# Kernel optimization log

Measured on AMD Instinct MI355X. Metric: run time of the kernel, lower is better.

Reference implementation:

```python
import jax, jax.numpy as jnp
import numpy as np

B, D, L, T, K = 16, 256, 256, 1000, 3
DW, DC = 4, 2  # dim_w, dim_c
CH = 8         # ConvSwishBlock out channels (10 = 1 start + 1 end + 8)


def swish(x):
    return x * jax.nn.sigmoid(x)


def setup_inputs() -> dict:
    key = jax.random.key(0)
    ks = jax.random.split(key, 12)
    # durations ~ U[1,6] per phone -> sum ~ 3.5*L ~ 896 <= T
    durations = 1.0 + 5.0 * jax.random.uniform(ks[0], (B, L), dtype=jnp.float32)
    phoneme = jax.random.normal(ks[1], (B, D, L), dtype=jnp.float32)
    # True = padded phone position
    phone_len = L - (jnp.arange(B) % 4) * 16
    phoneme_mask = (jnp.arange(L)[None, :] >= phone_len[:, None])[:, None, :]
    durations = jnp.where(phoneme_mask[:, 0, :], 0.0, durations)
    s = 0.02
    p = {
        'proj_w_W': s * jax.random.normal(ks[2], (D, D)), 'proj_w_b': jnp.zeros((D,)),
        'conv_w_W': s * jax.random.normal(ks[3], (CH, D, K)), 'conv_w_b': jnp.zeros((CH,)),
        'mlp_w_W': s * jax.random.normal(ks[4], (2 + CH, DW)), 'mlp_w_b': jnp.zeros((DW,)),
        'lin_w_W': s * jax.random.normal(ks[5], (D * DW, D)), 'lin_w_b': jnp.zeros((D,)),
        'proj_c_W': s * jax.random.normal(ks[6], (D, D)), 'proj_c_b': jnp.zeros((D,)),
        'conv_c_W': s * jax.random.normal(ks[7], (CH, D, K)), 'conv_c_b': jnp.zeros((CH,)),
        'mlp_c_W': s * jax.random.normal(ks[8], (2 + CH, DC)), 'mlp_c_b': jnp.zeros((DC,)),
        'lin_c_W': s * jax.random.normal(ks[9], (DW * DC, D)), 'lin_c_b': jnp.zeros((D,)),
    }
    return {'durations': durations, 'phoneme': phoneme, 'phoneme_mask': phoneme_mask, **p}


def _conv_branch(x, phone_pad, projW, projb, convW, convb):
    # x: (B, D, L). 1x1 conv projection, then K-wide 'same' conv to CH channels, swish, mask.
    x = jnp.einsum('od,bdl->bol', projW, x) + projb[None, :, None]
    h = jax.lax.conv_general_dilated(x, convW, (1,), 'SAME',
                                     dimension_numbers=('NCH', 'OIH', 'NCH'))
    h = swish(h + convb[None, :, None])
    h = jnp.where(phone_pad[:, None, :], 0.0, h)
    return h.transpose(0, 2, 1)  # (B, L, CH)


def _forward(durations, phoneme, phoneme_mask,
             proj_w_W, proj_w_b, conv_w_W, conv_w_b, mlp_w_W, mlp_w_b, lin_w_W, lin_w_b,
             proj_c_W, proj_c_b, conv_c_W, conv_c_b, mlp_c_W, mlp_c_b, lin_c_W, lin_c_b):
    phone_pad = phoneme_mask[:, 0, :]                       # (B, L) True = pad
    frame_len = jnp.clip(jnp.round(jnp.sum(durations, -1)), 0, T).astype(jnp.int32)
    frame_pad = jnp.arange(T)[None, :] >= frame_len[:, None]  # (B, T) True = pad
    attn_pad = frame_pad[:, :, None] | phone_pad[:, None, :]  # (B, T, L)

    sd = jnp.cumsum(durations, -1)                          # (B, L) cumulative end times
    sk = sd - durations                                     # (B, L) start times
    t = jnp.arange(1, T + 1, dtype=durations.dtype)
    S = jnp.where(attn_pad, 0.0, t[None, :, None] - sk[:, None, :])                    # (B,T,L)
    E = jnp.where(attn_pad, 0.0, jnp.broadcast_to(sd[:, None, :], attn_pad.shape)
                  - sk[:, None, :])                                                    # (B,T,L)

    # W branch: per-(frame, phone) attention weights over phones
    h_w = _conv_branch(phoneme, phone_pad, proj_w_W, proj_w_b, conv_w_W, conv_w_b)     # (B,L,CH)
    feat_w = jnp.concatenate(
        [S[..., None], E[..., None], jnp.broadcast_to(h_w[:, None], (B, T, L, CH))], -1)
    w = swish(feat_w @ mlp_w_W + mlp_w_b)                   # (B, T, L, DW)
    w = jnp.where(phone_pad[:, None, :, None], -jnp.inf, w)
    w = jax.nn.softmax(w, axis=2)                           # softmax over phones
    w = jnp.where(frame_pad[:, :, None, None], 0.0, w)

    # C branch: auxiliary per-(frame, phone) context
    h_c = _conv_branch(phoneme, phone_pad, proj_c_W, proj_c_b, conv_c_W, conv_c_b)
    feat_c = jnp.concatenate(
        [S[..., None], E[..., None], jnp.broadcast_to(h_c[:, None], (B, T, L, CH))], -1)
    c = swish(feat_c @ mlp_c_W + mlp_c_b)                   # (B, T, L, DC)

    # combine: wh = einsum over phones with phoneme features, wc with c matrix
    wh = jnp.einsum('btnq,bnh->btqh', w, phoneme.transpose(0, 2, 1))  # (B,T,DW,D)
    wh = wh.reshape(B, T, DW * D) @ lin_w_W + lin_w_b                 # (B,T,D)
    wc = jnp.einsum('btnq,btnp->btqp', w, c)                          # (B,T,DW,DC)
    wc = wc.reshape(B, T, DW * DC) @ lin_c_W + lin_c_b                # (B,T,D)
    return wh + wc


def reference(durations, phoneme, phoneme_mask,
              proj_w_W, proj_w_b, conv_w_W, conv_w_b, mlp_w_W, mlp_w_b, lin_w_W, lin_w_b,
              proj_c_W, proj_c_b, conv_c_W, conv_c_b, mlp_c_W, mlp_c_b, lin_c_W, lin_c_b):
    return _forward(durations, phoneme, phoneme_mask,
                    proj_w_W, proj_w_b, conv_w_W, conv_w_b, mlp_w_W, mlp_w_b, lin_w_W, lin_w_b,
                    proj_c_W, proj_c_b, conv_c_W, conv_c_b, mlp_c_W, mlp_c_b, lin_c_W, lin_c_b)
```

## Files before the change

kernel.cpp:

```cpp
#include <hip/hip_runtime.h>


typedef short v8s __attribute__((ext_vector_type(8)));
typedef float f4 __attribute__((ext_vector_type(4)));

__device__ __forceinline__ float bf2f(unsigned short h) {
  return __uint_as_float(((unsigned int)h) << 16);
}
__device__ __forceinline__ unsigned short f2bf(float f) {
  unsigned int u = __float_as_uint(f);
  u = (u + 0x7FFFu + ((u >> 16) & 1u)) >> 16;
  return (unsigned short)u;
}
__device__ __forceinline__ float swishf(float x) {
  return x * __builtin_amdgcn_rcpf(1.f + __expf(-x));
}

__global__ __launch_bounds__(256) void k_prep(
    const float* __restrict__ dur, const float* __restrict__ ph,
    const float* __restrict__ liWw,
    const float* __restrict__ cvWw, const float* __restrict__ pjWw,
    const float* __restrict__ pjbw,
    const float* __restrict__ cvWc, const float* __restrict__ pjWc,
    const float* __restrict__ pjbc,
    float* __restrict__ sk, int* __restrict__ frame_len,
    unsigned short* __restrict__ Mb, float* __restrict__ bK,
    unsigned short* __restrict__ LWT, unsigned short* __restrict__ phT) {
  __shared__ float sm[32 * 33];
  int blk = blockIdx.x, tid = threadIdx.x;
  if (blk < 16) {
    int b = blk, l = tid;
    float d = dur[b * 256 + l];
    sm[l] = d;
    __syncthreads();
    for (int off = 1; off < 256; off <<= 1) {
      float v = (l >= off) ? sm[l - off] : 0.f;
      __syncthreads();
      sm[l] += v;
      __syncthreads();
    }
    sk[b * 256 + l] = sm[l] - d;
    if (l == 255) {
      int fl = (int)rintf(sm[255]);
      frame_len[b] = min(max(fl, 0), 1000);
    }
  } else if (blk < 64) {
    int x = blk - 16;
    int br = x / 24, ck = x % 24;
    int ch = ck / 3, k = ck % 3;
    const float* convW = br ? cvWc : cvWw;
    const float* projW = br ? pjWc : pjWw;
    const float* projb = br ? pjbc : pjbw;
    int d = tid;
    float acc = 0.f;
    for (int o = 0; o < 256; o++)
      acc += convW[ch * 768 + o * 3 + k] * projW[o * 256 + d];
    Mb[(br * 24 + ck) * 256 + d] = f2bf(acc);
    if (d == 0) {
      float bb = 0.f;
      for (int o = 0; o < 256; o++)
        bb += convW[ch * 768 + o * 3 + k] * projb[o];
      bK[br * 24 + ck] = bb;
    }
  } else if (blk < 320) {
    int idx = blk - 64;
    int kt = idx & 31, ot = idx >> 5;
    int tx = tid & 31, ty = tid >> 5;
#pragma unroll
    for (int r = 0; r < 4; r++) {
      int row = ty + r * 8;
      sm[row * 33 + tx] = liWw[(size_t)(kt * 32 + row) * 256 + ot * 32 + tx];
    }
    __syncthreads();
#pragma unroll
    for (int r = 0; r < 4; r++) {
      int row = ty + r * 8;
      LWT[(size_t)(ot * 32 + row) * 1024 + kt * 32 + tx] =
          f2bf(sm[tx * 33 + row]);
    }
  } else {
    int idx = blk - 320;
    int ht = idx & 7, lt = (idx >> 3) & 7, b = idx >> 6;
    int tx = tid & 31, ty = tid >> 5;
#pragma unroll
    for (int r = 0; r < 4; r++) {
      int row = ty + r * 8;
      sm[row * 33 + tx] =
          ph[(size_t)b * 65536 + (size_t)(ht * 32 + row) * 256 + lt * 32 + tx];
    }
    __syncthreads();
#pragma unroll
    for (int r = 0; r < 4; r++) {
      int row = ty + r * 8;
      phT[(size_t)b * 65536 + (size_t)(lt * 32 + row) * 256 + ht * 32 + tx] =
          f2bf(sm[tx * 33 + row]);
    }
  }
}

__global__ __launch_bounds__(256) void k_conv(
    const unsigned short* __restrict__ phT, const unsigned short* __restrict__ Mb,
    const float* __restrict__ bK, const float* __restrict__ cvbw,
    const float* __restrict__ cvbc, const float* __restrict__ dur,
    float* __restrict__ hw, float* __restrict__ hc) {
  __shared__ float C[256 * 49];
  int b = blockIdx.x;
  int tid = threadIdx.x, wave = tid >> 6, lane = tid & 63;
  int quad = lane >> 4, col = lane & 15;
  int l0 = wave * 64;
  const unsigned short* Ab = phT + (size_t)b * 65536;
  f4 acc[4][3] = {};
#pragma unroll
  for (int k0 = 0; k0 < 256; k0 += 32) {
    v8s af[4], bf[3];
#pragma unroll
    for (int lt = 0; lt < 4; lt++)
      af[lt] = *(const v8s*)(Ab + (size_t)(l0 + lt * 16 + col) * 256 + k0 + quad * 8);
#pragma unroll
    for (int ct = 0; ct < 3; ct++)
      bf[ct] = *(const v8s*)(Mb + (size_t)(ct * 16 + col) * 256 + k0 + quad * 8);
#pragma unroll
    for (int lt = 0; lt < 4; lt++)
#pragma unroll
      for (int ct = 0; ct < 3; ct++)
        acc[lt][ct] = __builtin_amdgcn_mfma_f32_16x16x32_bf16(af[lt], bf[ct],
                                                              acc[lt][ct], 0, 0, 0);
  }
#pragma unroll
  for (int lt = 0; lt < 4; lt++)
#pragma unroll
    for (int ct = 0; ct < 3; ct++)
#pragma unroll
      for (int r = 0; r < 4; r++)
        C[(l0 + lt * 16 + quad * 4 + r) * 49 + ct * 16 + col] = acc[lt][ct][r];
  __syncthreads();
  int l = tid;
  float dv = dur[b * 256 + l];
  bool vld = (dv != 0.f);
#pragma unroll
  for (int br = 0; br < 2; br++) {
    const float* convb = br ? cvbc : cvbw;
    float* dst = br ? hc : hw;
#pragma unroll
    for (int ch = 0; ch < 8; ch++) {
      int ck = br * 24 + ch * 3;
      float v = convb[ch] + bK[ck + 1] + C[l * 49 + ck + 1];
      if (l > 0) v += bK[ck + 0] + C[(l - 1) * 49 + ck + 0];
      if (l < 255) v += bK[ck + 2] + C[(l + 1) * 49 + ck + 2];
      v = swishf(v);
      dst[((size_t)(b * 256 + l)) * 8 + ch] = vld ? v : 0.f;
    }
  }
}

__global__ __launch_bounds__(256) void k_wG(
    const unsigned short* __restrict__ LWT, const unsigned short* __restrict__ phT,
    const float* __restrict__ dur, const float* __restrict__ sk,
    const int* __restrict__ frame_len, const float* __restrict__ hw,
    const float* __restrict__ hc, const float* __restrict__ mlpWw,
    const float* __restrict__ mlpbw, const float* __restrict__ mlpWc,
    const float* __restrict__ mlpbc, unsigned short* __restrict__ G,
    unsigned short* __restrict__ wout, float* __restrict__ wcout) {
  __shared__ __align__(16) char smem[15360];
  int blk = blockIdx.x;
  int tid = threadIdx.x, wave = tid >> 6, lane = tid & 63;
  if (blk < 512) {
    int x = blk & 7, q = (blk >> 3) & 3, b = blk >> 5;
    int o0 = (x >> 1) * 64, l0 = (x & 1) * 128;
    int quad = lane >> 4, col = lane & 15;
    unsigned short* Asm = (unsigned short*)smem;
    unsigned short* Bsm = Asm + 64 * 40;
    int arow = wave * 16 + (lane >> 2);
    int aseg = lane & 3;
    const unsigned short* Ag = LWT + (size_t)(o0 + arow) * 1024 + q * 256 + aseg * 8;
    unsigned short* Al = Asm + arow * 40 + aseg * 8;
    int brow = wave * 32 + (lane >> 2);
    const unsigned short* Bg0 =
        phT + (size_t)b * 65536 + (size_t)(l0 + brow) * 256 + aseg * 8;
    const unsigned short* Bg1 = Bg0 + 16 * 256;
    unsigned short* Bl0 = Bsm + brow * 40 + aseg * 8;
    unsigned short* Bl1 = Bl0 + 16 * 40;
    int wm = (wave & 1) * 32, wn = (wave >> 1) * 64;
    f4 acc[2][4] = {};
    uint4 ra = *(const uint4*)Ag;
    uint4 rb0 = *(const uint4*)Bg0;
    uint4 rb1 = *(const uint4*)Bg1;
    for (int k0 = 0; k0 < 256; k0 += 32) {
      __syncthreads();
      *(uint4*)Al = ra;
      *(uint4*)Bl0 = rb0;
      *(uint4*)Bl1 = rb1;
      __syncthreads();
      if (k0 + 32 < 256) {
        ra = *(const uint4*)(Ag + k0 + 32);
        rb0 = *(const uint4*)(Bg0 + k0 + 32);
        rb1 = *(const uint4*)(Bg1 + k0 + 32);
      }
      v8s af[2], bf[4];
#pragma unroll
      for (int mt = 0; mt < 2; mt++)
        af[mt] = *(const v8s*)(Asm + (wm + mt * 16 + col) * 40 + quad * 8);
#pragma unroll
      for (int nt = 0; nt < 4; nt++)
        bf[nt] = *(const v8s*)(Bsm + (wn + nt * 16 + col) * 40 + quad * 8);
#pragma unroll
      for (int mt = 0; mt < 2; mt++)
#pragma unroll
        for (int nt = 0; nt < 4; nt++)
          acc[mt][nt] = __builtin_amdgcn_mfma_f32_16x16x32_bf16(af[mt], bf[nt],
                                                                acc[mt][nt], 0, 0, 0);
    }
    int quad2 = lane >> 4, col2 = lane & 15;
#pragma unroll
    for (int mt = 0; mt < 2; mt++)
#pragma unroll
      for (int nt = 0; nt < 4; nt++)
#pragma unroll
        for (int r = 0; r < 4; r++) {
          int orow = o0 + wm + mt * 16 + quad2 * 4 + r;
          int lcol = l0 + wn + nt * 16 + col2;
          G[(size_t)b * 262144 + (size_t)orow * 1024 + q * 256 + lcol] =
              f2bf(acc[mt][nt][r]);
        }
  } else {
    int idx = blk - 512;
    int b = idx >> 5;
    int tbase = (idx & 31) * 32 + wave * 8;
    int l0 = lane * 4;
    float mw[40], mbw[4], mc[20], mbc[2];
#pragma unroll
    for (int i = 0; i < 40; i++) mw[i] = mlpWw[i];
#pragma unroll
    for (int i = 0; i < 4; i++) mbw[i] = mlpbw[i];
#pragma unroll
    for (int i = 0; i < 20; i++) mc[i] = mlpWc[i];
#pragma unroll
    for (int i = 0; i < 2; i++) mbc[i] = mlpbc[i];
    float4 dv4 = *(const float4*)&dur[b * 256 + l0];
    float4 sk4 = *(const float4*)&sk[b * 256 + l0];
    float dv[4] = {dv4.x, dv4.y, dv4.z, dv4.w};
    float skv[4] = {sk4.x, sk4.y, sk4.z, sk4.w};
    bool val[4];
#pragma unroll
    for (int j = 0; j < 4; j++) val[j] = (dv[j] != 0.f);
    float hwv[4][8], hcv[4][8];
#pragma unroll
    for (int j = 0; j < 4; j++) {
      float4 a0 = *(const float4*)&hw[((size_t)(b * 256 + l0 + j)) * 8];
      float4 a1 = *(const float4*)&hw[((size_t)(b * 256 + l0 + j)) * 8 + 4];
      float4 c0 = *(const float4*)&hc[((size_t)(b * 256 + l0 + j)) * 8];
      float4 c1 = *(const float4*)&hc[((size_t)(b * 256 + l0 + j)) * 8 + 4];
      hwv[j][0] = a0.x; hwv[j][1] = a0.y; hwv[j][2] = a0.z; hwv[j][3] = a0.w;
      hwv[j][4] = a1.x; hwv[j][5] = a1.y; hwv[j][6] = a1.z; hwv[j][7] = a1.w;
      hcv[j][0] = c0.x; hcv[j][1] = c0.y; hcv[j][2] = c0.z; hcv[j][3] = c0.w;
      hcv[j][4] = c1.x; hcv[j][5] = c1.y; hcv[j][6] = c1.z; hcv[j][7] = c1.w;
    }
    float basew[4][4], basec[4][2];
#pragma unroll
    for (int j = 0; j < 4; j++) {
#pragma unroll
      for (int q = 0; q < 4; q++) {
        float a = mbw[q] + dv[j] * mw[4 + q];
#pragma unroll
        for (int ch = 0; ch < 8; ch++) a += hwv[j][ch] * mw[(2 + ch) * 4 + q];
        basew[j][q] = a;
      }
#pragma unroll
      for (int p = 0; p < 2; p++) {
        float a = mbc[p] + dv[j] * mc[2 + p];
#pragma unroll
        for (int ch = 0; ch < 8; ch++) a += hcv[j][ch] * mc[(2 + ch) * 2 + p];
        basec[j][p] = a;
      }
    }
    int fl = frame_len[b];
    for (int i = 0; i < 8; i++) {
      int t = tbase + i;
      if (t >= 1000) break;
      size_t wbase = ((size_t)(b * 1000 + t)) * 1024;
      if (t >= fl) {
        ushort4 z = {0, 0, 0, 0};
#pragma unroll
        for (int q = 0; q < 4; q++) *(ushort4*)(wout + wbase + q * 256 + l0) = z;
        if (lane == 0) {
          float4 fz = {0.f, 0.f, 0.f, 0.f};
          *(float4*)(wcout + ((size_t)(b * 1000 + t)) * 8) = fz;
          *(float4*)(wcout + ((size_t)(b * 1000 + t)) * 8 + 4) = fz;
        }
        continue;
      }
      float S[4];
#pragma unroll
      for (int j = 0; j < 4; j++) S[j] = (float)(t + 1) - skv[j];
      float lg[4][4];
#pragma unroll
      for (int j = 0; j < 4; j++)
#pragma unroll
        for (int q = 0; q < 4; q++)
          lg[j][q] = val[j] ? swishf(basew[j][q] + S[j] * mw[q]) : -INFINITY;
      float mx[4];
#pragma unroll
      for (int q = 0; q < 4; q++) {
        float v = fmaxf(fmaxf(lg[0][q], lg[1][q]), fmaxf(lg[2][q], lg[3][q]));
#pragma unroll
        for (int m = 1; m < 64; m <<= 1) v = fmaxf(v, __shfl_xor(v, m));
        mx[q] = v;
      }
      float e[4][4];
#pragma unroll
      for (int j = 0; j < 4; j++)
#pragma unroll
        for (int q = 0; q < 4; q++)
          e[j][q] = val[j] ? __expf(lg[j][q] - mx[q]) : 0.f;
      float inv[4];
#pragma unroll
      for (int q = 0; q < 4; q++) {
        float v = (e[0][q] + e[1][q]) + (e[2][q] + e[3][q]);
#pragma unroll
        for (int m = 1; m < 64; m <<= 1) v += __shfl_xor(v, m);
        inv[q] = __builtin_amdgcn_rcpf(v);
      }
      float w[4][4];
#pragma unroll
      for (int q = 0; q < 4; q++) {
        ushort4 o4;
        w[0][q] = e[0][q] * inv[q]; w[1][q] = e[1][q] * inv[q];
        w[2][q] = e[2][q] * inv[q]; w[3][q] = e[3][q] * inv[q];
        o4.x = f2bf(w[0][q]); o4.y = f2bf(w[1][q]);
        o4.z = f2bf(w[2][q]); o4.w = f2bf(w[3][q]);
        *(ushort4*)(wout + wbase + q * 256 + l0) = o4;
      }
      float cp[4][2];
#pragma unroll
      for (int j = 0; j < 4; j++)
#pragma unroll
        for (int p = 0; p < 2; p++)
          cp[j][p] = swishf(basec[j][p] + S[j] * mc[p]);
      float pr[8];
#pragma unroll
      for (int q = 0; q < 4; q++)
#pragma unroll
        for (int p = 0; p < 2; p++) {
          float v = w[0][q] * cp[0][p] + w[1][q] * cp[1][p] +
                    w[2][q] * cp[2][p] + w[3][q] * cp[3][p];
#pragma unroll
          for (int m = 1; m < 64; m <<= 1) v += __shfl_xor(v, m);
          pr[q * 2 + p] = v;
        }
      if (lane == 0) {
        float4 lo = {pr[0], pr[1], pr[2], pr[3]};
        float4 hi = {pr[4], pr[5], pr[6], pr[7]};
        *(float4*)(wcout + ((size_t)(b * 1000 + t)) * 8) = lo;
        *(float4*)(wcout + ((size_t)(b * 1000 + t)) * 8 + 4) = hi;
      }
    }
  }
}

__global__ __launch_bounds__(256) void k_gemmF(const unsigned short* __restrict__ wbuf,
                                               const unsigned short* __restrict__ G,
                                               const float* __restrict__ lwb,
                                               const float* __restrict__ lcb,
                                               const float* __restrict__ LC,
                                               const float* __restrict__ wc,
                                               float* __restrict__ out) {
  int b = blockIdx.y;
  int t0 = (blockIdx.x >> 1) * 64;
  int o0 = (blockIdx.x & 1) * 128;
  int tid = threadIdx.x, wave = tid >> 6, lane = tid & 63;
  int quad = lane >> 4, col = lane & 15;
  __shared__ __align__(16) unsigned short Asm[64 * 40];
  __shared__ __align__(16) unsigned short Bsm[128 * 40];
  __shared__ float bias_s[128];
  __shared__ float lcs[8][128];
  __shared__ float wcs[64][8];

  for (int i = tid; i < 128; i += 256) bias_s[i] = lwb[o0 + i] + lcb[o0 + i];
  for (int i = tid; i < 1024; i += 256)
    lcs[i >> 7][i & 127] = LC[(i >> 7) * 256 + o0 + (i & 127)];
  for (int i = tid; i < 512; i += 256) {
    int r = i >> 3, j = i & 7;
    int t = t0 + r;
    wcs[r][j] = (t < 1000) ? wc[((size_t)(b * 1000 + t)) * 8 + j] : 0.f;
  }

  int arow = wave * 16 + (lane >> 2);
  int aseg = lane & 3;
  const unsigned short* Ag =
      wbuf + (size_t)b * 1024000 + (size_t)(t0 + arow) * 1024 + aseg * 8;
  unsigned short* Al = Asm + arow * 40 + aseg * 8;
  int brow = wave * 32 + (lane >> 2);
  const unsigned short* Bg0 =
      G + (size_t)b * 262144 + (size_t)(o0 + brow) * 1024 + aseg * 8;
  const unsigned short* Bg1 = Bg0 + 16 * 1024;
  unsigned short* Bl0 = Bsm + brow * 40 + aseg * 8;
  unsigned short* Bl1 = Bl0 + 16 * 40;

  int wm = (wave & 1) * 32, wn = (wave >> 1) * 64;
  f4 acc[2][4] = {};
  uint4 ra = *(const uint4*)Ag;
  uint4 rb0 = *(const uint4*)Bg0;
  uint4 rb1 = *(const uint4*)Bg1;
  for (int k0 = 0; k0 < 1024; k0 += 32) {
    __syncthreads();
    *(uint4*)Al = ra;
    *(uint4*)Bl0 = rb0;
    *(uint4*)Bl1 = rb1;
    __syncthreads();
    if (k0 + 32 < 1024) {
      ra = *(const uint4*)(Ag + k0 + 32);
      rb0 = *(const uint4*)(Bg0 + k0 + 32);
      rb1 = *(const uint4*)(Bg1 + k0 + 32);
    }
    v8s af[2], bf[4];
#pragma unroll
    for (int mt = 0; mt < 2; mt++)
      af[mt] = *(const v8s*)(Asm + (wm + mt * 16 + col) * 40 + quad * 8);
#pragma unroll
    for (int nt = 0; nt < 4; nt++)
      bf[nt] = *(const v8s*)(Bsm + (wn + nt * 16 + col) * 40 + quad * 8);
#pragma unroll
    for (int mt = 0; mt < 2; mt++)
#pragma unroll
      for (int nt = 0; nt < 4; nt++)
        acc[mt][nt] = __builtin_amdgcn_mfma_f32_16x16x32_bf16(af[mt], bf[nt],
                                                              acc[mt][nt], 0, 0, 0);
  }
#pragma unroll
  for (int mt = 0; mt < 2; mt++)
#pragma unroll
    for (int r = 0; r < 4; r++) {
      int lrow = wm + mt * 16 + quad * 4 + r;
      int trow = t0 + lrow;
      if (trow < 1000) {
        float wcl[8];
        float4 wa = *(const float4*)&wcs[lrow][0];
        float4 wb = *(const float4*)&wcs[lrow][4];
        wcl[0] = wa.x; wcl[1] = wa.y; wcl[2] = wa.z; wcl[3] = wa.w;
        wcl[4] = wb.x; wcl[5] = wb.y; wcl[6] = wb.z; wcl[7] = wb.w;
#pragma unroll
        for (int nt = 0; nt < 4; nt++) {
          int oc = wn + nt * 16 + col;
          float v = acc[mt][nt][r] + bias_s[oc];
#pragma unroll
          for (int jj = 0; jj < 8; jj++) v = fmaf(wcl[jj], lcs[jj][oc], v);
          out[((size_t)(b * 1000 + trow)) * 256 + o0 + oc] = v;
        }
      }
    }
}

extern "C" void kernel_launch(void* const* d_in, const int* in_sizes, int n_in,
                              void* d_out, int out_size, void* d_ws, size_t ws_size,
                              hipStream_t stream) {
  const float* dur  = (const float*)d_in[0];
  const float* ph   = (const float*)d_in[1];
  const float* pjWw = (const float*)d_in[3];
  const float* pjbw = (const float*)d_in[4];
  const float* cvWw = (const float*)d_in[5];
  const float* cvbw = (const float*)d_in[6];
  const float* mlWw = (const float*)d_in[7];
  const float* mlbw = (const float*)d_in[8];
  const float* liWw = (const float*)d_in[9];
  const float* libw = (const float*)d_in[10];
  const float* pjWc = (const float*)d_in[11];
  const float* pjbc = (const float*)d_in[12];
  const float* cvWc = (const float*)d_in[13];
  const float* cvbc = (const float*)d_in[14];
  const float* mlWc = (const float*)d_in[15];
  const float* mlbc = (const float*)d_in[16];
  const float* liWc = (const float*)d_in[17];
  const float* libc = (const float*)d_in[18];
  float* out = (float*)d_out;

  float* f = (float*)d_ws;
  size_t o = 0;
  float* sk = f + o;            o += 4096;
  int* fl = (int*)(f + o);      o += 16;
  float* bK = f + o;            o += 64;
  unsigned short* Mb = (unsigned short*)(f + o); o += 6144;
  float* hw = f + o;            o += 16 * 256 * 8;
  float* hc = f + o;            o += 16 * 256 * 8;
  float* wc = f + o;            o += 16 * 1000 * 8;
  unsigned short* wbuf = (unsigned short*)(f + o); o += 8224768;
  unsigned short* G    = (unsigned short*)(f + o); o += 2097152;
  unsigned short* phT  = (unsigned short*)(f + o); o += 524288;
  unsigned short* LWT  = (unsigned short*)(f + o); o += 131072;

  k_prep<<<1344, 256, 0, stream>>>(dur, ph, liWw, cvWw, pjWw, pjbw, cvWc, pjWc,
                                   pjbc, sk, fl, Mb, bK, LWT, phT);
  k_conv<<<16, 256, 0, stream>>>(phT, Mb, bK, cvbw, cvbc, dur, hw, hc);
  k_wG<<<1024, 256, 0, stream>>>(LWT, phT, dur, sk, fl, hw, hc, mlWw, mlbw,
                                 mlWc, mlbc, G, wbuf, wc);
  k_gemmF<<<dim3(32, 16), 256, 0, stream>>>(wbuf, G, libw, libc, liWc, wc, out);
}
```

Baseline: 187.9 us.

## Fuse softmax weight generation into final GEMM, merge conv with G GEMM

The softmax attention weights are now computed per t-tile inside the final GEMM kernel and staged as unnormalized bf16 exponentials in shared memory. Per-row normalization is applied after each q-slice GEMM, so the large bf16 weight buffer is no longer written to and read back from global memory. The conv kernel and the G GEMM are merged into one launch, which cuts the launch count and lets the two run concurrently. In exchange, each of the two o-tiles for a given t-range recomputes the softmax, and the kernel uses more shared memory and issues more syncs per block.

```diff
diff --git a/kernel.cpp b/kernel.cpp
--- a/kernel.cpp
+++ b/kernel.cpp
@@ -98,76 +98,68 @@
   }
 }
 
-__global__ __launch_bounds__(256) void k_conv(
+__global__ __launch_bounds__(256) void k_convG(
     const unsigned short* __restrict__ phT, const unsigned short* __restrict__ Mb,
     const float* __restrict__ bK, const float* __restrict__ cvbw,
     const float* __restrict__ cvbc, const float* __restrict__ dur,
-    float* __restrict__ hw, float* __restrict__ hc) {
-  __shared__ float C[256 * 49];
-  int b = blockIdx.x;
+    const unsigned short* __restrict__ LWT,
+    float* __restrict__ hw, float* __restrict__ hc,
+    unsigned short* __restrict__ G) {
+  __shared__ __align__(16) char smem[50176];
+  int blk = blockIdx.x;
   int tid = threadIdx.x, wave = tid >> 6, lane = tid & 63;
   int quad = lane >> 4, col = lane & 15;
-  int l0 = wave * 64;
-  const unsigned short* Ab = phT + (size_t)b * 65536;
-  f4 acc[4][3] = {};
-#pragma unroll
-  for (int k0 = 0; k0 < 256; k0 += 32) {
-    v8s af[4], bf[3];
+  if (blk < 16) {
+    float* C = (float*)smem;
+    int b = blk;
+    int l0 = wave * 64;
+    const unsigned short* Ab = phT + (size_t)b * 65536;
+    f4 acc[4][3] = {};
+#pragma unroll
+    for (int k0 = 0; k0 < 256; k0 += 32) {
+      v8s af[4], bf[3];
+#pragma unroll
+      for (int lt = 0; lt < 4; lt++)
+        af[lt] = *(const v8s*)(Ab + (size_t)(l0 + lt * 16 + col) * 256 + k0 + quad * 8);
+#pragma unroll
+      for (int ct = 0; ct < 3; ct++)
+        bf[ct] = *(const v8s*)(Mb + (size_t)(ct * 16 + col) * 256 + k0 + quad * 8);
+#pragma unroll
+      for (int lt = 0; lt < 4; lt++)
+#pragma unroll
+        for (int ct = 0; ct < 3; ct++)
+          acc[lt][ct] = __builtin_amdgcn_mfma_f32_16x16x32_bf16(af[lt], bf[ct],
+                                                                acc[lt][ct], 0, 0, 0);
+    }
 #pragma unroll
     for (int lt = 0; lt < 4; lt++)
-      af[lt] = *(const v8s*)(Ab + (size_t)(l0 + lt * 16 + col) * 256 + k0 + quad * 8);
-#pragma unroll
-    for (int ct = 0; ct < 3; ct++)
-      bf[ct] = *(const v8s*)(Mb + (size_t)(ct * 16 + col) * 256 + k0 + quad * 8);
-#pragma unroll
-    for (int lt = 0; lt < 4; lt++)
 #pragma unroll
       for (int ct = 0; ct < 3; ct++)
-        acc[lt][ct] = __builtin_amdgcn_mfma_f32_16x16x32_bf16(af[lt], bf[ct],
-                                                              acc[lt][ct], 0, 0, 0);
-  }
-#pragma unroll
-  for (int lt = 0; lt < 4; lt++)
-#pragma unroll
-    for (int ct = 0; ct < 3; ct++)
-#pragma unroll
-      for (int r = 0; r < 4; r++)
-        C[(l0 + lt * 16 + quad * 4 + r) * 49 + ct * 16 + col] = acc[lt][ct][r];
-  __syncthreads();
-  int l = tid;
-  float dv = dur[b * 256 + l];
-  bool vld = (dv != 0.f);
-#pragma unroll
-  for (int br = 0; br < 2; br++) {
-    const float* convb = br ? cvbc : cvbw;
-    float* dst = br ? hc : hw;
-#pragma unroll
-    for (int ch = 0; ch < 8; ch++) {
-      int ck = br * 24 + ch * 3;
-      float v = convb[ch] + bK[ck + 1] + C[l * 49 + ck + 1];
-      if (l > 0) v += bK[ck + 0] + C[(l - 1) * 49 + ck + 0];
-      if (l < 255) v += bK[ck + 2] + C[(l + 1) * 49 + ck + 2];
-      v = swishf(v);
-      dst[((size_t)(b * 256 + l)) * 8 + ch] = vld ? v : 0.f;
-    }
-  }
-}
-
-__global__ __launch_bounds__(256) void k_wG(
-    const unsigned short* __restrict__ LWT, const unsigned short* __restrict__ phT,
-    const float* __restrict__ dur, const float* __restrict__ sk,
-    const int* __restrict__ frame_len, const float* __restrict__ hw,
-    const float* __restrict__ hc, const float* __restrict__ mlpWw,
-    const float* __restrict__ mlpbw, const float* __restrict__ mlpWc,
-    const float* __restrict__ mlpbc, unsigned short* __restrict__ G,
-    unsigned short* __restrict__ wout, float* __restrict__ wcout) {
-  __shared__ __align__(16) char smem[15360];
-  int blk = blockIdx.x;
-  int tid = threadIdx.x, wave = tid >> 6, lane = tid & 63;
-  if (blk < 512) {
-    int x = blk & 7, q = (blk >> 3) & 3, b = blk >> 5;
+#pragma unroll
+        for (int r = 0; r < 4; r++)
+          C[(l0 + lt * 16 + quad * 4 + r) * 49 + ct * 16 + col] = acc[lt][ct][r];
+    __syncthreads();
+    int l = tid;
+    float dv = dur[b * 256 + l];
+    bool vld = (dv != 0.f);
+#pragma unroll
+    for (int br = 0; br < 2; br++) {
+      const float* convb = br ? cvbc : cvbw;
+      float* dst = br ? hc : hw;
+#pragma unroll
+      for (int ch = 0; ch < 8; ch++) {
+        int ck = br * 24 + ch * 3;
+        float v = convb[ch] + bK[ck + 1] + C[l * 49 + ck + 1];
+        if (l > 0) v += bK[ck + 0] + C[(l - 1) * 49 + ck + 0];
+        if (l < 255) v += bK[ck + 2] + C[(l + 1) * 49 + ck + 2];
+        v = swishf(v);
+        dst[((size_t)(b * 256 + l)) * 8 + ch] = vld ? v : 0.f;
+      }
+    }
+  } else {
+    int idx = blk - 16;
+    int x = idx & 7, q = (idx >> 3) & 3, b = idx >> 5;
     int o0 = (x >> 1) * 64, l0 = (x & 1) * 128;
-    int quad = lane >> 4, col = lane & 15;
     unsigned short* Asm = (unsigned short*)smem;
     unsigned short* Bsm = Asm + 64 * 40;
     int arow = wave * 16 + (lane >> 2);
@@ -210,222 +202,170 @@
           acc[mt][nt] = __builtin_amdgcn_mfma_f32_16x16x32_bf16(af[mt], bf[nt],
                                                                 acc[mt][nt], 0, 0, 0);
     }
-    int quad2 = lane >> 4, col2 = lane & 15;
 #pragma unroll
     for (int mt = 0; mt < 2; mt++)
 #pragma unroll
       for (int nt = 0; nt < 4; nt++)
 #pragma unroll
         for (int r = 0; r < 4; r++) {
-          int orow = o0 + wm + mt * 16 + quad2 * 4 + r;
-          int lcol = l0 + wn + nt * 16 + col2;
+          int orow = o0 + wm + mt * 16 + quad * 4 + r;
+          int lcol = l0 + wn + nt * 16 + col;
           G[(size_t)b * 262144 + (size_t)orow * 1024 + q * 256 + lcol] =
               f2bf(acc[mt][nt][r]);
         }
-  } else {
-    int idx = blk - 512;
-    int b = idx >> 5;
-    int tbase = (idx & 31) * 32 + wave * 8;
-    int l0 = lane * 4;
-    float mw[40], mbw[4], mc[20], mbc[2];
-#pragma unroll
-    for (int i = 0; i < 40; i++) mw[i] = mlpWw[i];
-#pragma unroll
-    for (int i = 0; i < 4; i++) mbw[i] = mlpbw[i];
-#pragma unroll
-    for (int i = 0; i < 20; i++) mc[i] = mlpWc[i];
-#pragma unroll
-    for (int i = 0; i < 2; i++) mbc[i] = mlpbc[i];
-    float4 dv4 = *(const float4*)&dur[b * 256 + l0];
-    float4 sk4 = *(const float4*)&sk[b * 256 + l0];
-    float dv[4] = {dv4.x, dv4.y, dv4.z, dv4.w};
-    float skv[4] = {sk4.x, sk4.y, sk4.z, sk4.w};
-    bool val[4];
-#pragma unroll
-    for (int j = 0; j < 4; j++) val[j] = (dv[j] != 0.f);
-    float hwv[4][8], hcv[4][8];
-#pragma unroll
-    for (int j = 0; j < 4; j++) {
-      float4 a0 = *(const float4*)&hw[((size_t)(b * 256 + l0 + j)) * 8];
-      float4 a1 = *(const float4*)&hw[((size_t)(b * 256 + l0 + j)) * 8 + 4];
-      float4 c0 = *(const float4*)&hc[((size_t)(b * 256 + l0 + j)) * 8];
-      float4 c1 = *(const float4*)&hc[((size_t)(b * 256 + l0 + j)) * 8 + 4];
-      hwv[j][0] = a0.x; hwv[j][1] = a0.y; hwv[j][2] = a0.z; hwv[j][3] = a0.w;
-      hwv[j][4] = a1.x; hwv[j][5] = a1.y; hwv[j][6] = a1.z; hwv[j][7] = a1.w;
-      hcv[j][0] = c0.x; hcv[j][1] = c0.y; hcv[j][2] = c0.z; hcv[j][3] = c0.w;
-      hcv[j][4] = c1.x; hcv[j][5] = c1.y; hcv[j][6] = c1.z; hcv[j][7] = c1.w;
-    }
-    float basew[4][4], basec[4][2];
-#pragma unroll
-    for (int j = 0; j < 4; j++) {
-#pragma unroll
-      for (int q = 0; q < 4; q++) {
-        float a = mbw[q] + dv[j] * mw[4 + q];
-#pragma unroll
-        for (int ch = 0; ch < 8; ch++) a += hwv[j][ch] * mw[(2 + ch) * 4 + q];
-        basew[j][q] = a;
-      }
-#pragma unroll
-      for (int p = 0; p < 2; p++) {
-        float a = mbc[p] + dv[j] * mc[2 + p];
-#pragma unroll
-        for (int ch = 0; ch < 8; ch++) a += hcv[j][ch] * mc[(2 + ch) * 2 + p];
-        basec[j][p] = a;
-      }
-    }
-    int fl = frame_len[b];
-    for (int i = 0; i < 8; i++) {
-      int t = tbase + i;
-      if (t >= 1000) break;
-      size_t wbase = ((size_t)(b * 1000 + t)) * 1024;
-      if (t >= fl) {
-        ushort4 z = {0, 0, 0, 0};
-#pragma unroll
-        for (int q = 0; q < 4; q++) *(ushort4*)(wout + wbase + q * 256 + l0) = z;
-        if (lane == 0) {
-          float4 fz = {0.f, 0.f, 0.f, 0.f};
-          *(float4*)(wcout + ((size_t)(b * 1000 + t)) * 8) = fz;
-          *(float4*)(wcout + ((size_t)(b * 1000 + t)) * 8 + 4) = fz;
-        }
-        continue;
-      }
-      float S[4];
-#pragma unroll
-      for (int j = 0; j < 4; j++) S[j] = (float)(t + 1) - skv[j];
-      float lg[4][4];
-#pragma unroll
-      for (int j = 0; j < 4; j++)
-#pragma unroll
-        for (int q = 0; q < 4; q++)
-          lg[j][q] = val[j] ? swishf(basew[j][q] + S[j] * mw[q]) : -INFINITY;
-      float mx[4];
-#pragma unroll
-      for (int q = 0; q < 4; q++) {
-        float v = fmaxf(fmaxf(lg[0][q], lg[1][q]), fmaxf(lg[2][q], lg[3][q]));
-#pragma unroll
-        for (int m = 1; m < 64; m <<= 1) v = fmaxf(v, __shfl_xor(v, m));
-        mx[q] = v;
-      }
-      float e[4][4];
-#pragma unroll
-      for (int j = 0; j < 4; j++)
-#pragma unroll
-        for (int q = 0; q < 4; q++)
-          e[j][q] = val[j] ? __expf(lg[j][q] - mx[q]) : 0.f;
-      float inv[4];
-#pragma unroll
-      for (int q = 0; q < 4; q++) {
-        float v = (e[0][q] + e[1][q]) + (e[2][q] + e[3][q]);
-#pragma unroll
-        for (int m = 1; m < 64; m <<= 1) v += __shfl_xor(v, m);
-        inv[q] = __builtin_amdgcn_rcpf(v);
-      }
-      float w[4][4];
-#pragma unroll
-      for (int q = 0; q < 4; q++) {
-        ushort4 o4;
-        w[0][q] = e[0][q] * inv[q]; w[1][q] = e[1][q] * inv[q];
-        w[2][q] = e[2][q] * inv[q]; w[3][q] = e[3][q] * inv[q];
-        o4.x = f2bf(w[0][q]); o4.y = f2bf(w[1][q]);
-        o4.z = f2bf(w[2][q]); o4.w = f2bf(w[3][q]);
-        *(ushort4*)(wout + wbase + q * 256 + l0) = o4;
-      }
-      float cp[4][2];
-#pragma unroll
-      for (int j = 0; j < 4; j++)
-#pragma unroll
-        for (int p = 0; p < 2; p++)
-          cp[j][p] = swishf(basec[j][p] + S[j] * mc[p]);
-      float pr[8];
-#pragma unroll
-      for (int q = 0; q < 4; q++)
-#pragma unroll
-        for (int p = 0; p < 2; p++) {
-          float v = w[0][q] * cp[0][p] + w[1][q] * cp[1][p] +
-                    w[2][q] * cp[2][p] + w[3][q] * cp[3][p];
-#pragma unroll
-          for (int m = 1; m < 64; m <<= 1) v += __shfl_xor(v, m);
-          pr[q * 2 + p] = v;
-        }
-      if (lane == 0) {
-        float4 lo = {pr[0], pr[1], pr[2], pr[3]};
-        float4 hi = {pr[4], pr[5], pr[6], pr[7]};
-        *(float4*)(wcout + ((size_t)(b * 1000 + t)) * 8) = lo;
-        *(float4*)(wcout + ((size_t)(b * 1000 + t)) * 8 + 4) = hi;
-      }
-    }
   }
 }
 
-__global__ __launch_bounds__(256) void k_gemmF(const unsigned short* __restrict__ wbuf,
-                                               const unsigned short* __restrict__ G,
-                                               const float* __restrict__ lwb,
-                                               const float* __restrict__ lcb,
-                                               const float* __restrict__ LC,
-                                               const float* __restrict__ wc,
-                                               float* __restrict__ out) {
-  int b = blockIdx.y;
-  int t0 = (blockIdx.x >> 1) * 64;
-  int o0 = (blockIdx.x & 1) * 128;
+__global__ __launch_bounds__(256) void k_fuse(
+    const unsigned short* __restrict__ G,
+    const float* __restrict__ dur, const float* __restrict__ sk,
+    const int* __restrict__ frame_len,
+    const float* __restrict__ hw, const float* __restrict__ hc,
+    const float* __restrict__ mlpWw, const float* __restrict__ mlpbw,
+    const float* __restrict__ mlpWc, const float* __restrict__ mlpbc,
+    const float* __restrict__ lwb, const float* __restrict__ lcb,
+    const float* __restrict__ LC, float* __restrict__ out) {
+  __shared__ __align__(16) unsigned short Etile[64 * 264];
+  __shared__ __align__(16) unsigned short Bsm[128 * 40];
+  __shared__ float Lbw[256 * 4];
+  __shared__ float Laux[256 * 4];
+  __shared__ float invL[64 * 4];
+  __shared__ float wcL[64 * 8];
+  __shared__ float bias_s[128];
+  __shared__ float lcs[8 * 128];
+
+  int blk = blockIdx.x;
+  int b = (blk & 7) * 2 + ((blk >> 3) >> 5);
+  int tile = (blk >> 3) & 31;
+  int t0 = (tile >> 1) * 64;
+  int o0 = (tile & 1) * 128;
   int tid = threadIdx.x, wave = tid >> 6, lane = tid & 63;
   int quad = lane >> 4, col = lane & 15;
-  __shared__ __align__(16) unsigned short Asm[64 * 40];
-  __shared__ __align__(16) unsigned short Bsm[128 * 40];
-  __shared__ float bias_s[128];
-  __shared__ float lcs[8][128];
-  __shared__ float wcs[64][8];
-
+
+  {
+    int l = tid;
+    float4 a0 = *(const float4*)&hw[((size_t)(b * 256 + l)) * 8];
+    float4 a1 = *(const float4*)&hw[((size_t)(b * 256 + l)) * 8 + 4];
+    float4 c0 = *(const float4*)&hc[((size_t)(b * 256 + l)) * 8];
+    float4 c1 = *(const float4*)&hc[((size_t)(b * 256 + l)) * 8 + 4];
+    float hwv[8] = {a0.x, a0.y, a0.z, a0.w, a1.x, a1.y, a1.z, a1.w};
+    float hcv[8] = {c0.x, c0.y, c0.z, c0.w, c1.x, c1.y, c1.z, c1.w};
+    float dl = dur[b * 256 + l];
+    float skl = sk[b * 256 + l];
+#pragma unroll
+    for (int q = 0; q < 4; q++) {
+      float a = mlpbw[q] + dl * mlpWw[4 + q];
+#pragma unroll
+      for (int ch = 0; ch < 8; ch++) a += hwv[ch] * mlpWw[(2 + ch) * 4 + q];
+      Lbw[l * 4 + q] = a;
+    }
+    float bc0 = mlpbc[0] + dl * mlpWc[2];
+    float bc1 = mlpbc[1] + dl * mlpWc[3];
+#pragma unroll
+    for (int ch = 0; ch < 8; ch++) {
+      bc0 += hcv[ch] * mlpWc[(2 + ch) * 2 + 0];
+      bc1 += hcv[ch] * mlpWc[(2 + ch) * 2 + 1];
+    }
+    Laux[l * 4 + 0] = bc0;
+    Laux[l * 4 + 1] = bc1;
+    Laux[l * 4 + 2] = skl;
+    Laux[l * 4 + 3] = (dl != 0.f) ? 1.f : 0.f;
+  }
   for (int i = tid; i < 128; i += 256) bias_s[i] = lwb[o0 + i] + lcb[o0 + i];
   for (int i = tid; i < 1024; i += 256)
-    lcs[i >> 7][i & 127] = LC[(i >> 7) * 256 + o0 + (i & 127)];
-  for (int i = tid; i < 512; i += 256) {
-    int r = i >> 3, j = i & 7;
-    int t = t0 + r;
-    wcs[r][j] = (t < 1000) ? wc[((size_t)(b * 1000 + t)) * 8 + j] : 0.f;
+    lcs[(i >> 7) * 128 + (i & 127)] = LC[(i >> 7) * 256 + o0 + (i & 127)];
+
+  float mwS[4] = {mlpWw[0], mlpWw[1], mlpWw[2], mlpWw[3]};
+  float mcS0 = mlpWc[0], mcS1 = mlpWc[1];
+  int fl = frame_len[b];
+  int tl = tid >> 2, seg = tid & 3;
+  int t = t0 + tl;
+  bool live = (t < fl);
+  float tp1 = (float)(t + 1);
+
+  int wm = (wave & 1) * 32, wn = (wave >> 1) * 64;
+  int brow = wave * 32 + (lane >> 2), bseg = lane & 3;
+  f4 accF[2][4] = {};
+
+  for (int q = 0; q < 4; q++) {
+    __syncthreads();
+    float mwq = mwS[q];
+    float m = -INFINITY;
+    if (live) {
+      for (int j = 0; j < 64; j++) {
+        int l = seg * 64 + ((j + (seg << 4)) & 63);
+        float4 aux = *(const float4*)&Laux[l * 4];
+        float S = tp1 - aux.z;
+        float lg = (aux.w != 0.f) ? swishf(Lbw[l * 4 + q] + S * mwq) : -INFINITY;
+        m = fmaxf(m, lg);
+      }
+    }
+    m = fmaxf(m, __shfl_xor(m, 1));
+    m = fmaxf(m, __shfl_xor(m, 2));
+    float s = 0.f, e0 = 0.f, e1 = 0.f;
+    for (int j = 0; j < 64; j++) {
+      int l = seg * 64 + ((j + (seg << 4)) & 63);
+      float4 aux = *(const float4*)&Laux[l * 4];
+      float S = tp1 - aux.z;
+      float lg = (aux.w != 0.f) ? swishf(Lbw[l * 4 + q] + S * mwq) : -INFINITY;
+      float e = live ? __expf(lg - m) : 0.f;
+      float cp0 = swishf(aux.x + S * mcS0);
+      float cp1 = swishf(aux.y + S * mcS1);
+      s += e;
+      e0 += e * cp0;
+      e1 += e * cp1;
+      Etile[tl * 264 + l] = f2bf(e);
+    }
+    s += __shfl_xor(s, 1);  e0 += __shfl_xor(e0, 1);  e1 += __shfl_xor(e1, 1);
+    s += __shfl_xor(s, 2);  e0 += __shfl_xor(e0, 2);  e1 += __shfl_xor(e1, 2);
+    if (seg == 0) {
+      float iv = live ? __builtin_amdgcn_rcpf(s) : 0.f;
+      invL[tl * 4 + q] = iv;
+      wcL[tl * 8 + q * 2 + 0] = e0 * iv;
+      wcL[tl * 8 + q * 2 + 1] = e1 * iv;
+    }
+    const unsigned short* Bg0 =
+        G + (size_t)b * 262144 + (size_t)(o0 + brow) * 1024 + q * 256 + bseg * 8;
+    const unsigned short* Bg1 = Bg0 + 16 * 1024;
+    unsigned short* Bl0 = Bsm + brow * 40 + bseg * 8;
+    unsigned short* Bl1 = Bl0 + 16 * 40;
+    f4 accq[2][4] = {};
+    uint4 rb0 = *(const uint4*)Bg0;
+    uint4 rb1 = *(const uint4*)Bg1;
+    for (int k0 = 0; k0 < 256; k0 += 32) {
+      __syncthreads();
+      *(uint4*)Bl0 = rb0;
+      *(uint4*)Bl1 = rb1;
+      __syncthreads();
+      if (k0 + 32 < 256) {
+        rb0 = *(const uint4*)(Bg0 + k0 + 32);
+        rb1 = *(const uint4*)(Bg1 + k0 + 32);
+      }
+      v8s af[2], bf[4];
+#pragma unroll
+      for (int mt = 0; mt < 2; mt++)
+        af[mt] = *(const v8s*)(Etile + (wm + mt * 16 + col) * 264 + k0 + quad * 8);
+#pragma unroll
+      for (int nt = 0; nt < 4; nt++)
+        bf[nt] = *(const v8s*)(Bsm + (wn + nt * 16 + col) * 40 + quad * 8);
+#pragma unroll
+      for (int mt = 0; mt < 2; mt++)
+#pragma unroll
+        for (int nt = 0; nt < 4; nt++)
+          accq[mt][nt] = __builtin_amdgcn_mfma_f32_16x16x32_bf16(af[mt], bf[nt],
+                                                                 accq[mt][nt], 0, 0, 0);
+    }
+#pragma unroll
+    for (int mt = 0; mt < 2; mt++)
+#pragma unroll
+      for (int r = 0; r < 4; r++) {
+        float iv = invL[(wm + mt * 16 + quad * 4 + r) * 4 + q];
+#pragma unroll
+        for (int nt = 0; nt < 4; nt++)
+          accF[mt][nt][r] += accq[mt][nt][r] * iv;
+      }
   }
 
-  int arow = wave * 16 + (lane >> 2);
-  int aseg = lane & 3;
-  const unsigned short* Ag =
-      wbuf + (size_t)b * 1024000 + (size_t)(t0 + arow) * 1024 + aseg * 8;
-  unsigned short* Al = Asm + arow * 40 + aseg * 8;
-  int brow = wave * 32 + (lane >> 2);
-  const unsigned short* Bg0 =
-      G + (size_t)b * 262144 + (size_t)(o0 + brow) * 1024 + aseg * 8;
-  const unsigned short* Bg1 = Bg0 + 16 * 1024;
-  unsigned short* Bl0 = Bsm + brow * 40 + aseg * 8;
-  unsigned short* Bl1 = Bl0 + 16 * 40;
-
-  int wm = (wave & 1) * 32, wn = (wave >> 1) * 64;
-  f4 acc[2][4] = {};
-  uint4 ra = *(const uint4*)Ag;
-  uint4 rb0 = *(const uint4*)Bg0;
-  uint4 rb1 = *(const uint4*)Bg1;
-  for (int k0 = 0; k0 < 1024; k0 += 32) {
-    __syncthreads();
-    *(uint4*)Al = ra;
-    *(uint4*)Bl0 = rb0;
-    *(uint4*)Bl1 = rb1;
-    __syncthreads();
-    if (k0 + 32 < 1024) {
-      ra = *(const uint4*)(Ag + k0 + 32);
-      rb0 = *(const uint4*)(Bg0 + k0 + 32);
-      rb1 = *(const uint4*)(Bg1 + k0 + 32);
-    }
-    v8s af[2], bf[4];
-#pragma unroll
-    for (int mt = 0; mt < 2; mt++)
-      af[mt] = *(const v8s*)(Asm + (wm + mt * 16 + col) * 40 + quad * 8);
-#pragma unroll
-    for (int nt = 0; nt < 4; nt++)
-      bf[nt] = *(const v8s*)(Bsm + (wn + nt * 16 + col) * 40 + quad * 8);
-#pragma unroll
-    for (int mt = 0; mt < 2; mt++)
-#pragma unroll
-      for (int nt = 0; nt < 4; nt++)
-        acc[mt][nt] = __builtin_amdgcn_mfma_f32_16x16x32_bf16(af[mt], bf[nt],
-                                                              acc[mt][nt], 0, 0, 0);
-  }
 #pragma unroll
   for (int mt = 0; mt < 2; mt++)
 #pragma unroll
@@ -433,17 +373,15 @@
       int lrow = wm + mt * 16 + quad * 4 + r;
       int trow = t0 + lrow;
       if (trow < 1000) {
-        float wcl[8];
-        float4 wa = *(const float4*)&wcs[lrow][0];
-        float4 wb = *(const float4*)&wcs[lrow][4];
-        wcl[0] = wa.x; wcl[1] = wa.y; wcl[2] = wa.z; wcl[3] = wa.w;
-        wcl[4] = wb.x; wcl[5] = wb.y; wcl[6] = wb.z; wcl[7] = wb.w;
+        float4 wa = *(const float4*)&wcL[lrow * 8];
+        float4 wb = *(const float4*)&wcL[lrow * 8 + 4];
+        float wcl[8] = {wa.x, wa.y, wa.z, wa.w, wb.x, wb.y, wb.z, wb.w};
 #pragma unroll
         for (int nt = 0; nt < 4; nt++) {
           int oc = wn + nt * 16 + col;
-          float v = acc[mt][nt][r] + bias_s[oc];
-#pragma unroll
-          for (int jj = 0; jj < 8; jj++) v = fmaf(wcl[jj], lcs[jj][oc], v);
+          float v = accF[mt][nt][r] + bias_s[oc];
+#pragma unroll
+          for (int jj = 0; jj < 8; jj++) v = fmaf(wcl[jj], lcs[jj * 128 + oc], v);
           out[((size_t)(b * 1000 + trow)) * 256 + o0 + oc] = v;
         }
       }
@@ -481,16 +419,13 @@
   unsigned short* Mb = (unsigned short*)(f + o); o += 6144;
   float* hw = f + o;            o += 16 * 256 * 8;
   float* hc = f + o;            o += 16 * 256 * 8;
-  float* wc = f + o;            o += 16 * 1000 * 8;
-  unsigned short* wbuf = (unsigned short*)(f + o); o += 8224768;
-  unsigned short* G    = (unsigned short*)(f + o); o += 2097152;
-  unsigned short* phT  = (unsigned short*)(f + o); o += 524288;
-  unsigned short* LWT  = (unsigned short*)(f + o); o += 131072;
+  unsigned short* G   = (unsigned short*)(f + o); o += 2097152;
+  unsigned short* phT = (unsigned short*)(f + o); o += 524288;
+  unsigned short* LWT = (unsigned short*)(f + o); o += 131072;
 
   k_prep<<<1344, 256, 0, stream>>>(dur, ph, liWw, cvWw, pjWw, pjbw, cvWc, pjWc,
                                    pjbc, sk, fl, Mb, bK, LWT, phT);
-  k_conv<<<16, 256, 0, stream>>>(phT, Mb, bK, cvbw, cvbc, dur, hw, hc);
-  k_wG<<<1024, 256, 0, stream>>>(LWT, phT, dur, sk, fl, hw, hc, mlWw, mlbw,
-                                 mlWc, mlbc, G, wbuf, wc);
-  k_gemmF<<<dim3(32, 16), 256, 0, stream>>>(wbuf, G, libw, libc, liWc, wc, out);
-}
+  k_convG<<<528, 256, 0, stream>>>(phT, Mb, bK, cvbw, cvbc, dur, LWT, hw, hc, G);
+  k_fuse<<<512, 256, 0, stream>>>(G, dur, sk, fl, hw, hc, mlWw, mlbw, mlWc,
+                                  mlbc, libw, libc, liWc, out);
+}
```

Result: slower. 234.1 us (+24.6%).
